# Performance work log

Measured on AMD Instinct MI355X. Metric: run time of the kernel, lower is better.

The kernel has to match this reference:

```python
import jax, jax.numpy as jnp
import numpy as np

TEMPERATURE = 0.07
NORMALIZE = True
NEG_INF = -1e30


def setup_inputs() -> dict:
    key = jax.random.key(0)
    features = jax.random.normal(key, (8192, 512), dtype=jnp.float32)
    return {"features": features}


def reference(features):
    # features: [B, D]
    B = features.shape[0]
    if NORMALIZE:
        norm = jnp.linalg.norm(features, axis=1, keepdims=True)
        features = features / jnp.maximum(norm, 1e-12)
    # [B, B] similarity matrix
    sim = jnp.matmul(features, features.T) / TEMPERATURE

    # default SimCLR labels: arange(B//2) repeated twice -> pair (i, i + B//2)
    half = jnp.arange(B // 2, dtype=jnp.int32)
    labels = jnp.concatenate([half, half])
    eq = labels[None, :] == labels[:, None]          # [B, B]
    diag = jnp.eye(B, dtype=bool)
    mask_pos = eq & ~diag                            # positives per row

    # Original per-row CE: logits = cat(pos_sims, neg_sims) (= all j != i),
    # target index 0 = FIRST positive (lowest column index). Loss_i =
    # logsumexp_{j != i}(sim[i, j]) - sim[i, first_pos_i].
    sim_masked = jnp.where(diag, NEG_INF, sim)
    lse = jax.scipy.special.logsumexp(sim_masked, axis=1)   # [B]

    first_pos = jnp.argmax(mask_pos, axis=1)                 # first True per row
    pos_sim = jnp.take_along_axis(sim, first_pos[:, None], axis=1)[:, 0]

    has_pos = jnp.any(mask_pos, axis=1)
    losses = jnp.where(has_pos, lse - pos_sim, 0.0)
    count = jnp.maximum(jnp.sum(has_pos.astype(jnp.float32)), 1.0)
    return jnp.sum(losses) / count
```

## Files before the change

### kernel.cpp

```cpp
#include <hip/hip_runtime.h>
#include <hip/hip_bf16.h>
#include <stdint.h>

#define BATCH 8192
#define DIM   512
#define TILE  128
#define BK    64
#define NT    (BATCH / TILE)
#define NPAIR (NT * (NT + 1) / 2)

#define FEAT_SCALE 4.5398164f
#define LN2        0.69314718055994531f

typedef __attribute__((ext_vector_type(8))) short short8;
typedef __attribute__((ext_vector_type(4))) float f32x4;

__device__ __forceinline__ void gld_lds16(const void* g, void* l) {
  __builtin_amdgcn_global_load_lds(
      (__attribute__((address_space(1))) void*)(uintptr_t)g,
      (__attribute__((address_space(3))) void*)(uintptr_t)l,
      16, 0, 0);
}

__global__ __launch_bounds__(256) void normalize_bf16(
    const float* __restrict__ x, __hip_bfloat16* __restrict__ o,
    float* __restrict__ rowsum) {
  const int wv = threadIdx.x >> 6, lane = threadIdx.x & 63;
  const int row = blockIdx.x * 4 + wv;
  if (lane == 0) rowsum[row] = 0.0f;
  const float4* xr = (const float4*)(x + (size_t)row * DIM);
  const float4 v0 = xr[lane];
  const float4 v1 = xr[lane + 64];
  float ss = v0.x * v0.x + v0.y * v0.y + v0.z * v0.z + v0.w * v0.w +
             v1.x * v1.x + v1.y * v1.y + v1.z * v1.z + v1.w * v1.w;
#pragma unroll
  for (int m = 32; m > 0; m >>= 1) ss += __shfl_xor(ss, m, 64);
  const float inv = FEAT_SCALE / fmaxf(sqrtf(ss), 1e-12f);
  ushort4 p0, p1;
  p0.x = __bfloat16_as_ushort(__float2bfloat16(v0.x * inv));
  p0.y = __bfloat16_as_ushort(__float2bfloat16(v0.y * inv));
  p0.z = __bfloat16_as_ushort(__float2bfloat16(v0.z * inv));
  p0.w = __bfloat16_as_ushort(__float2bfloat16(v0.w * inv));
  p1.x = __bfloat16_as_ushort(__float2bfloat16(v1.x * inv));
  p1.y = __bfloat16_as_ushort(__float2bfloat16(v1.y * inv));
  p1.z = __bfloat16_as_ushort(__float2bfloat16(v1.z * inv));
  p1.w = __bfloat16_as_ushort(__float2bfloat16(v1.w * inv));
  ushort4* orow = (ushort4*)(o + (size_t)row * DIM);
  orow[lane]      = p0;
  orow[lane + 64] = p1;
}

__global__ __launch_bounds__(256, 4) void sim_lse_kernel(
    const __hip_bfloat16* __restrict__ F, float* __restrict__ rowsum,
    float* __restrict__ possim) {
  __shared__ __hip_bfloat16 smem[2 * TILE * BK];
  __shared__ float colAcc[TILE];

  const int t = blockIdx.x;
  int by = (int)((129.0f - sqrtf(129.0f * 129.0f - 8.0f * (float)t)) * 0.5f);
  if (by > NT - 1) by = NT - 1;
  if (by < 0) by = 0;
  while ((by + 1) * (129 - (by + 1)) / 2 <= t) ++by;
  while (by * (129 - by) / 2 > t) --by;
  const int bx = by + (t - by * (129 - by) / 2);
  const bool diagTile = (bx == by);

  const int rowBase = by * TILE;
  const int colBase = bx * TILE;

  const int tid   = threadIdx.x;
  const int lane  = tid & 63;
  const int wv    = tid >> 6;
  const int waveM = wv >> 1;
  const int waveN = wv & 1;
  const int quad  = lane >> 4;
  const int l15   = lane & 15;

  if (tid < TILE) colAcc[tid] = 0.0f;

  f32x4 acc[4][4] = {};

  const int sb = lane & 7;
  const __hip_bfloat16* gA[4];
  const __hip_bfloat16* gB[4];
  char* ldsA[4];
  char* ldsB[4];
#pragma unroll
  for (int c = 0; c < 4; ++c) {
    const int sRow = wv * 32 + c * 8 + (lane >> 3);
    const int g = sb ^ (sRow & 7);
    gA[c] = F + (size_t)(rowBase + sRow) * DIM + g * 8;
    gB[c] = F + (size_t)(colBase + sRow) * DIM + g * 8;
    ldsA[c] = (char*)smem + (wv * 4 + c) * 1024;
    ldsB[c] = (char*)smem + 16384 + (wv * 4 + c) * 1024;
  }

  int aOff[4], bOff[4];
#pragma unroll
  for (int i = 0; i < 4; ++i) {
    const int Ra = waveM * 64 + i * 16 + l15;
    aOff[i] = Ra * 128 + (quad ^ (Ra & 7)) * 16;
    const int Rb = waveN * 64 + i * 16 + l15;
    bOff[i] = 16384 + Rb * 128 + (quad ^ (Rb & 7)) * 16;
  }
  char* sbase = (char*)smem;

  for (int k0 = 0; k0 < DIM; k0 += BK) {
#pragma unroll
    for (int c = 0; c < 4; ++c) {
      gld_lds16(gA[c] + k0, ldsA[c]);
      gld_lds16(gB[c] + k0, ldsB[c]);
    }
    __syncthreads();

    short8 a[4], b[4];
#pragma unroll
    for (int i = 0; i < 4; ++i) {
      a[i] = *(const short8*)(sbase + aOff[i]);
      b[i] = *(const short8*)(sbase + bOff[i]);
    }
#pragma unroll
    for (int mi = 0; mi < 4; ++mi)
#pragma unroll
      for (int ni = 0; ni < 4; ++ni)
        acc[mi][ni] =
            __builtin_amdgcn_mfma_f32_16x16x32_bf16(a[mi], b[ni], acc[mi][ni], 0, 0, 0);
#pragma unroll
    for (int i = 0; i < 4; ++i) {
      a[i] = *(const short8*)(sbase + (aOff[i] ^ 64));
      b[i] = *(const short8*)(sbase + (bOff[i] ^ 64));
    }
#pragma unroll
    for (int mi = 0; mi < 4; ++mi)
#pragma unroll
      for (int ni = 0; ni < 4; ++ni)
        acc[mi][ni] =
            __builtin_amdgcn_mfma_f32_16x16x32_bf16(a[mi], b[ni], acc[mi][ni], 0, 0, 0);
    __syncthreads();
  }

  float* redBuf = (float*)smem;
  f32x4 rsumv[4] = {};
  float colpart[4] = {0.0f, 0.0f, 0.0f, 0.0f};

  if (diagTile) {
#pragma unroll
    for (int mi = 0; mi < 4; ++mi)
#pragma unroll
      for (int ni = 0; ni < 4; ++ni)
#pragma unroll
        for (int r = 0; r < 4; ++r) {
          const int rl = waveM * 64 + mi * 16 + quad * 4 + r;
          const int cl = waveN * 64 + ni * 16 + l15;
          rsumv[mi][r] += (cl == rl) ? 0.0f : exp2f(acc[mi][ni][r]);
        }
  } else {
    const bool hasPos = (bx == by + 32);
#pragma unroll
    for (int mi = 0; mi < 4; ++mi)
#pragma unroll
      for (int ni = 0; ni < 4; ++ni)
#pragma unroll
        for (int r = 0; r < 4; ++r) {
          const float s = acc[mi][ni][r];
          const float e = exp2f(s);
          rsumv[mi][r] += e;
          colpart[ni] += e;
          if (hasPos) {
            const int rl = waveM * 64 + mi * 16 + quad * 4 + r;
            const int cl = waveN * 64 + ni * 16 + l15;
            if (cl == rl) {
              const int gi = rowBase + rl;
              possim[gi] = s;
              possim[gi + 4096] = s;
            }
          }
        }
  }

  {
    float* wbase = redBuf + ((waveN * 2 + waveM) * 16 + l15) * 68 + quad * 4;
#pragma unroll
    for (int mi = 0; mi < 4; ++mi)
      *(f32x4*)(wbase + mi * 16) = rsumv[mi];
  }

  if (!diagTile) {
#pragma unroll
    for (int ni = 0; ni < 4; ++ni) {
      float c = colpart[ni];
      c += __shfl_xor(c, 16, 64);
      c += __shfl_xor(c, 32, 64);
      if (quad == 0) atomicAdd(&colAcc[waveN * 64 + ni * 16 + l15], c);
    }
  }
  __syncthreads();

  {
    const int wn = tid >> 7, r = tid & 127;
    const int strip = r >> 6, rl = r & 63;
    const float* base = redBuf + ((wn * 2 + strip) * 16) * 68 + rl;
    float s = 0.0f;
#pragma unroll
    for (int j = 0; j < 16; ++j) s += base[j * 68];
    atomicAdd(&rowsum[rowBase + r], s);
  }
  if (tid < TILE && !diagTile)
    atomicAdd(&rowsum[colBase + tid], colAcc[tid]);
}

__global__ __launch_bounds__(1024) void finalize_kernel(
    const float* __restrict__ rowsum, const float* __restrict__ possim,
    float* __restrict__ out) {
  float acc = 0.0f;
  for (int i = threadIdx.x; i < BATCH; i += 1024)
    acc += __logf(rowsum[i]) - possim[i] * LN2;
#pragma unroll
  for (int m = 32; m > 0; m >>= 1) acc += __shfl_xor(acc, m, 64);
  __shared__ float ws[16];
  const int lane = threadIdx.x & 63, wv = threadIdx.x >> 6;
  if (lane == 0) ws[wv] = acc;
  __syncthreads();
  if (threadIdx.x == 0) {
    float tot = 0.0f;
#pragma unroll
    for (int k = 0; k < 16; ++k) tot += ws[k];
    out[0] = tot * (1.0f / (float)BATCH);
  }
}

extern "C" void kernel_launch(void* const* d_in, const int* in_sizes, int n_in,
                              void* d_out, int out_size, void* d_ws, size_t ws_size,
                              hipStream_t stream) {
  const float* x = (const float*)d_in[0];
  float* out = (float*)d_out;

  __hip_bfloat16* Fb = (__hip_bfloat16*)d_ws;
  float* rowsum = (float*)((char*)d_ws + (size_t)BATCH * DIM * sizeof(__hip_bfloat16));
  float* possim = rowsum + BATCH;

  normalize_bf16<<<BATCH / 4, 256, 0, stream>>>(x, Fb, rowsum);
  sim_lse_kernel<<<NPAIR, 256, 0, stream>>>(Fb, rowsum, possim);
  finalize_kernel<<<1, 1024, 0, stream>>>(rowsum, possim, out);
}
```

Before: 112.4 us.

## Use 256x256 tiles with an explicitly pipelined multi-buffered LDS main loop

Doubles the similarity tile to 256x256 and processes it with 512 threads and 8x4 MFMA accumulators per wave, so each loaded row block is reused more and fewer triangular tiles are launched. The K loop is fully unrolled into a hand-scheduled pipeline. Asynchronous global-to-LDS loads for later K slices are issued while MFMAs run on the current slice, using raw s_barrier, vmcnt waits and setprio. The pipeline needs about 129 KB of dynamic LDS, which limits occupancy to one block per CU, and leaves only 528 blocks, which risks load imbalance across CUs.

```diff
diff --git a/kernel.cpp b/kernel.cpp
--- a/kernel.cpp
+++ b/kernel.cpp
@@ -4,9 +4,9 @@
 
 #define BATCH 8192
 #define DIM   512
-#define TILE  128
+#define BM    256
 #define BK    64
-#define NT    (BATCH / TILE)
+#define NT    (BATCH / BM)
 #define NPAIR (NT * (NT + 1) / 2)
 
 #define FEAT_SCALE 4.5398164f
@@ -50,162 +50,178 @@
   orow[lane + 64] = p1;
 }
 
-__global__ __launch_bounds__(256, 4) void sim_lse_kernel(
+__global__ __launch_bounds__(512, 2) void sim_lse_kernel(
     const __hip_bfloat16* __restrict__ F, float* __restrict__ rowsum,
     float* __restrict__ possim) {
-  __shared__ __hip_bfloat16 smem[2 * TILE * BK];
-  __shared__ float colAcc[TILE];
+  extern __shared__ char smem[];
+  float* colAcc = (float*)(smem + 131072);
 
   const int t = blockIdx.x;
-  int by = (int)((129.0f - sqrtf(129.0f * 129.0f - 8.0f * (float)t)) * 0.5f);
+  int by = (int)((65.0f - sqrtf(65.0f * 65.0f - 8.0f * (float)t)) * 0.5f);
   if (by > NT - 1) by = NT - 1;
   if (by < 0) by = 0;
-  while ((by + 1) * (129 - (by + 1)) / 2 <= t) ++by;
-  while (by * (129 - by) / 2 > t) --by;
-  const int bx = by + (t - by * (129 - by) / 2);
+  while ((by + 1) * (65 - (by + 1)) / 2 <= t) ++by;
+  while (by * (65 - by) / 2 > t) --by;
+  const int bx = by + (t - by * (65 - by) / 2);
   const bool diagTile = (bx == by);
-
-  const int rowBase = by * TILE;
-  const int colBase = bx * TILE;
-
-  const int tid   = threadIdx.x;
-  const int lane  = tid & 63;
-  const int wv    = tid >> 6;
-  const int waveM = wv >> 1;
-  const int waveN = wv & 1;
-  const int quad  = lane >> 4;
-  const int l15   = lane & 15;
-
-  if (tid < TILE) colAcc[tid] = 0.0f;
-
-  f32x4 acc[4][4] = {};
-
-  const int sb = lane & 7;
-  const __hip_bfloat16* gA[4];
-  const __hip_bfloat16* gB[4];
-  char* ldsA[4];
-  char* ldsB[4];
-#pragma unroll
-  for (int c = 0; c < 4; ++c) {
-    const int sRow = wv * 32 + c * 8 + (lane >> 3);
-    const int g = sb ^ (sRow & 7);
-    gA[c] = F + (size_t)(rowBase + sRow) * DIM + g * 8;
-    gB[c] = F + (size_t)(colBase + sRow) * DIM + g * 8;
-    ldsA[c] = (char*)smem + (wv * 4 + c) * 1024;
-    ldsB[c] = (char*)smem + 16384 + (wv * 4 + c) * 1024;
-  }
-
-  int aOff[4], bOff[4];
-#pragma unroll
-  for (int i = 0; i < 4; ++i) {
-    const int Ra = waveM * 64 + i * 16 + l15;
-    aOff[i] = Ra * 128 + (quad ^ (Ra & 7)) * 16;
-    const int Rb = waveN * 64 + i * 16 + l15;
-    bOff[i] = 16384 + Rb * 128 + (quad ^ (Rb & 7)) * 16;
-  }
-  char* sbase = (char*)smem;
-
-  for (int k0 = 0; k0 < DIM; k0 += BK) {
-#pragma unroll
-    for (int c = 0; c < 4; ++c) {
-      gld_lds16(gA[c] + k0, ldsA[c]);
-      gld_lds16(gB[c] + k0, ldsB[c]);
+  const bool hasPos = (bx == by + NT / 2);
+
+  const int rowBase = by * BM;
+  const int colBase = bx * BM;
+
+  const int tid  = threadIdx.x;
+  const int lane = tid & 63;
+  const int wv   = tid >> 6;
+  const int q    = lane >> 4;
+  const int l15  = lane & 15;
+  const int waveM = wv >> 2;
+  const int waveN = wv & 3;
+
+  const int r0 = tid >> 2, s0 = tid & 3;
+  const int r1 = (tid + 512) >> 2;
+  const __hip_bfloat16* gA0 = F + (size_t)(rowBase + r0) * DIM + (s0 ^ (r0 & 3)) * 8;
+  const __hip_bfloat16* gA1 = F + (size_t)(rowBase + r1) * DIM + (s0 ^ (r1 & 3)) * 8;
+  const __hip_bfloat16* gB0 = F + (size_t)(colBase + r0) * DIM + (s0 ^ (r0 & 3)) * 8;
+  const __hip_bfloat16* gB1 = F + (size_t)(colBase + r1) * DIM + (s0 ^ (r1 & 3)) * 8;
+  char* ldsW0 = smem + wv * 1024;
+  char* ldsW1 = ldsW0 + 8192;
+
+  const int aoff = waveM * 8192 + l15 * 64 + ((q ^ (l15 & 3)) * 16);
+  const int boff = waveN * 4096 + l15 * 64 + ((q ^ (l15 & 3)) * 16);
+  const char* sA = smem;
+  const char* sB = smem + 65536;
+
+  if (tid < 256) colAcc[tid] = 0.0f;
+
+  f32x4 acc[8][4] = {};
+  short8 a[4], b0[4], b1[4];
+
+#define BARRIER() asm volatile("s_barrier" ::: "memory")
+#define VMCNT4()  asm volatile("s_waitcnt vmcnt(4)" ::: "memory")
+#define SP1() __builtin_amdgcn_s_setprio(1)
+#define SP0() __builtin_amdgcn_s_setprio(0)
+
+#define STAGE(T_, KK_, ISB_) do {                                             \
+    const __hip_bfloat16* g0_ = (ISB_) ? gB0 : gA0;                           \
+    const __hip_bfloat16* g1_ = (ISB_) ? gB1 : gA1;                           \
+    const int ko_ = ((T_) & 7) * BK + (KK_) * 32;                             \
+    const int pl_ = ((((T_) & 1) * 2 + (KK_)) << 14) + ((ISB_) ? 65536 : 0);  \
+    gld_lds16(g0_ + ko_, ldsW0 + pl_);                                        \
+    gld_lds16(g1_ + ko_, ldsW1 + pl_);                                        \
+  } while (0)
+
+#define LDA4(PK_, H_) do {                                                    \
+    const char* p_ = sA + ((PK_) << 14) + aoff + (H_) * 4096;                 \
+    a[0] = *(const short8*)(p_);                                              \
+    a[1] = *(const short8*)(p_ + 1024);                                       \
+    a[2] = *(const short8*)(p_ + 2048);                                       \
+    a[3] = *(const short8*)(p_ + 3072);                                       \
+  } while (0)
+
+#define LDB4(PK_, BV_) do {                                                   \
+    const char* p_ = sB + ((PK_) << 14) + boff;                               \
+    BV_[0] = *(const short8*)(p_);                                            \
+    BV_[1] = *(const short8*)(p_ + 1024);                                     \
+    BV_[2] = *(const short8*)(p_ + 2048);                                     \
+    BV_[3] = *(const short8*)(p_ + 3072);                                     \
+  } while (0)
+
+#define MFMA16(H_, BV_) do {                                                  \
+    _Pragma("unroll")                                                         \
+    for (int m_ = 0; m_ < 4; ++m_)                                            \
+      _Pragma("unroll")                                                       \
+      for (int n_ = 0; n_ < 4; ++n_)                                          \
+        acc[(H_) * 4 + m_][n_] = __builtin_amdgcn_mfma_f32_16x16x32_bf16(     \
+            a[m_], BV_[n_], acc[(H_) * 4 + m_][n_], 0, 0, 0);                 \
+  } while (0)
+
+#define ITER(U_, V_) do {                                                     \
+     LDA4(0, 0); LDB4(0, b0); STAGE((V_), 1, 0);                     \
+    BARRIER(); SP1(); MFMA16(0, b0); SP0(); BARRIER();                        \
+     LDA4(0, 1); STAGE((V_), 1, 1);                                  \
+    BARRIER(); SP1(); MFMA16(1, b0); SP0(); BARRIER();                        \
+     LDA4(1, 0); LDB4(1, b1); STAGE((U_) + 2, 0, 0);                 \
+    BARRIER(); SP1(); MFMA16(0, b1); SP0(); BARRIER();                        \
+     LDA4(1, 1); STAGE((U_) + 2, 0, 1); VMCNT4();                    \
+    BARRIER(); SP1(); MFMA16(1, b1); SP0(); BARRIER();                        \
+     LDA4(2, 0); LDB4(2, b0); STAGE((U_) + 2, 1, 0);                 \
+    BARRIER(); SP1(); MFMA16(0, b0); SP0(); BARRIER();                        \
+     LDA4(2, 1); STAGE((U_) + 2, 1, 1);                              \
+    BARRIER(); SP1(); MFMA16(1, b0); SP0(); BARRIER();                        \
+     LDA4(3, 0); LDB4(3, b1); STAGE((V_) + 2, 0, 0);                 \
+    BARRIER(); SP1(); MFMA16(0, b1); SP0(); BARRIER();                        \
+     LDA4(3, 1); STAGE((V_) + 2, 0, 1); VMCNT4();                    \
+    BARRIER(); SP1(); MFMA16(1, b1); SP0(); BARRIER();                        \
+  } while (0)
+
+  STAGE(0, 0, 0); STAGE(0, 0, 1); STAGE(0, 1, 0); STAGE(0, 1, 1);
+  STAGE(1, 0, 0); STAGE(1, 0, 1);
+  asm volatile("s_waitcnt vmcnt(4) lgkmcnt(0)" ::: "memory");
+  BARRIER();
+
+  ITER(0, 1);
+  ITER(2, 3);
+  ITER(4, 5);
+  ITER(6, 7);
+
+  asm volatile("s_waitcnt vmcnt(0)" ::: "memory");
+  BARRIER();
+
+  float* redBuf = (float*)smem;
+  float cp[4] = {0.f, 0.f, 0.f, 0.f};
+  f32x4 rp[8];
+
+#pragma unroll
+  for (int mi = 0; mi < 8; ++mi) {
+    f32x4 r = {0.f, 0.f, 0.f, 0.f};
+#pragma unroll
+    for (int ni = 0; ni < 4; ++ni) {
+      const int lc = waveN * 64 + ni * 16 + l15;
+#pragma unroll
+      for (int rr = 0; rr < 4; ++rr) {
+        const int lr = waveM * 128 + mi * 16 + q * 4 + rr;
+        const float s = acc[mi][ni][rr];
+        float e = exp2f(s);
+        if (diagTile && lc == lr) e = 0.0f;
+        r[rr] += e;
+        cp[ni] += e;
+        if (hasPos && lc == lr) {
+          const int gi = rowBase + lr;
+          possim[gi] = s;
+          possim[gi + BATCH / 2] = s;
+        }
+      }
     }
-    __syncthreads();
-
-    short8 a[4], b[4];
-#pragma unroll
-    for (int i = 0; i < 4; ++i) {
-      a[i] = *(const short8*)(sbase + aOff[i]);
-      b[i] = *(const short8*)(sbase + bOff[i]);
-    }
-#pragma unroll
-    for (int mi = 0; mi < 4; ++mi)
-#pragma unroll
-      for (int ni = 0; ni < 4; ++ni)
-        acc[mi][ni] =
-            __builtin_amdgcn_mfma_f32_16x16x32_bf16(a[mi], b[ni], acc[mi][ni], 0, 0, 0);
-#pragma unroll
-    for (int i = 0; i < 4; ++i) {
-      a[i] = *(const short8*)(sbase + (aOff[i] ^ 64));
-      b[i] = *(const short8*)(sbase + (bOff[i] ^ 64));
-    }
-#pragma unroll
-    for (int mi = 0; mi < 4; ++mi)
-#pragma unroll
-      for (int ni = 0; ni < 4; ++ni)
-        acc[mi][ni] =
-            __builtin_amdgcn_mfma_f32_16x16x32_bf16(a[mi], b[ni], acc[mi][ni], 0, 0, 0);
-    __syncthreads();
-  }
-
-  float* redBuf = (float*)smem;
-  f32x4 rsumv[4] = {};
-  float colpart[4] = {0.0f, 0.0f, 0.0f, 0.0f};
-
-  if (diagTile) {
-#pragma unroll
-    for (int mi = 0; mi < 4; ++mi)
-#pragma unroll
-      for (int ni = 0; ni < 4; ++ni)
-#pragma unroll
-        for (int r = 0; r < 4; ++r) {
-          const int rl = waveM * 64 + mi * 16 + quad * 4 + r;
-          const int cl = waveN * 64 + ni * 16 + l15;
-          rsumv[mi][r] += (cl == rl) ? 0.0f : exp2f(acc[mi][ni][r]);
-        }
-  } else {
-    const bool hasPos = (bx == by + 32);
-#pragma unroll
-    for (int mi = 0; mi < 4; ++mi)
-#pragma unroll
-      for (int ni = 0; ni < 4; ++ni)
-#pragma unroll
-        for (int r = 0; r < 4; ++r) {
-          const float s = acc[mi][ni][r];
-          const float e = exp2f(s);
-          rsumv[mi][r] += e;
-          colpart[ni] += e;
-          if (hasPos) {
-            const int rl = waveM * 64 + mi * 16 + quad * 4 + r;
-            const int cl = waveN * 64 + ni * 16 + l15;
-            if (cl == rl) {
-              const int gi = rowBase + rl;
-              possim[gi] = s;
-              possim[gi + 4096] = s;
-            }
-          }
-        }
+    rp[mi] = r;
   }
 
   {
-    float* wbase = redBuf + ((waveN * 2 + waveM) * 16 + l15) * 68 + quad * 4;
-#pragma unroll
-    for (int mi = 0; mi < 4; ++mi)
-      *(f32x4*)(wbase + mi * 16) = rsumv[mi];
+    float* wb = redBuf + (waveN * 16 + l15) * 260 + waveM * 128 + q * 4;
+#pragma unroll
+    for (int mi = 0; mi < 8; ++mi) *(f32x4*)(wb + mi * 16) = rp[mi];
   }
 
   if (!diagTile) {
 #pragma unroll
     for (int ni = 0; ni < 4; ++ni) {
-      float c = colpart[ni];
+      float c = cp[ni];
       c += __shfl_xor(c, 16, 64);
       c += __shfl_xor(c, 32, 64);
-      if (quad == 0) atomicAdd(&colAcc[waveN * 64 + ni * 16 + l15], c);
+      if (q == 0) atomicAdd(&colAcc[waveN * 64 + ni * 16 + l15], c);
     }
   }
-  __syncthreads();
+  asm volatile("s_waitcnt lgkmcnt(0)" ::: "memory");
+  BARRIER();
 
   {
-    const int wn = tid >> 7, r = tid & 127;
-    const int strip = r >> 6, rl = r & 63;
-    const float* base = redBuf + ((wn * 2 + strip) * 16) * 68 + rl;
-    float s = 0.0f;
-#pragma unroll
-    for (int j = 0; j < 16; ++j) s += base[j * 68];
-    atomicAdd(&rowsum[rowBase + r], s);
-  }
-  if (tid < TILE && !diagTile)
+    const int row = tid >> 1, half = tid & 1;
+    const float* bp = redBuf + (half * 32) * 260 + row;
+    float ssum = 0.f;
+#pragma unroll
+    for (int j = 0; j < 32; ++j) ssum += bp[j * 260];
+    atomicAdd(&rowsum[rowBase + row], ssum);
+  }
+  if (!diagTile && tid < 256)
     atomicAdd(&rowsum[colBase + tid], colAcc[tid]);
 }
 
@@ -239,7 +255,14 @@
   float* rowsum = (float*)((char*)d_ws + (size_t)BATCH * DIM * sizeof(__hip_bfloat16));
   float* possim = rowsum + BATCH;
 
+  static bool attr_done = false;
+  if (!attr_done) {
+    (void)hipFuncSetAttribute(reinterpret_cast<const void*>(sim_lse_kernel),
+                              hipFuncAttributeMaxDynamicSharedMemorySize, 132096);
+    attr_done = true;
+  }
+
   normalize_bf16<<<BATCH / 4, 256, 0, stream>>>(x, Fb, rowsum);
-  sim_lse_kernel<<<NPAIR, 256, 0, stream>>>(Fb, rowsum, possim);
+  sim_lse_kernel<<<NPAIR, 512, 132096, stream>>>(Fb, rowsum, possim);
   finalize_kernel<<<1, 1024, 0, stream>>>(rowsum, possim, out);
 }
```

Measured after the change: 136.6 us. 21.5% more time.

## Fuse finalize reduction into sim kernel via last-block atomic counter

Applied to the files above, without the earlier changes.

Removes the separate finalize kernel launch. Positive similarities are now summed per tile into a single global accumulator, and the last block to finish, found through an atomic counter with a threadfence, computes the log-sum over row sums and writes the loss. This saves one launch and the per-row possim buffer. In exchange it adds a global atomic and a fence to every block, and the tail reduction runs serially in one 256-thread block.

```diff
diff --git a/kernel.cpp b/kernel.cpp
--- a/kernel.cpp
+++ b/kernel.cpp
@@ -24,10 +24,12 @@
 
 __global__ __launch_bounds__(256) void normalize_bf16(
     const float* __restrict__ x, __hip_bfloat16* __restrict__ o,
-    float* __restrict__ rowsum) {
+    float* __restrict__ rowsum, float* __restrict__ possimSum,
+    int* __restrict__ counter) {
   const int wv = threadIdx.x >> 6, lane = threadIdx.x & 63;
   const int row = blockIdx.x * 4 + wv;
   if (lane == 0) rowsum[row] = 0.0f;
+  if (blockIdx.x == 0 && threadIdx.x == 0) { *possimSum = 0.0f; *counter = 0; }
   const float4* xr = (const float4*)(x + (size_t)row * DIM);
   const float4 v0 = xr[lane];
   const float4 v1 = xr[lane + 64];
@@ -52,9 +54,12 @@
 
 __global__ __launch_bounds__(256, 4) void sim_lse_kernel(
     const __hip_bfloat16* __restrict__ F, float* __restrict__ rowsum,
-    float* __restrict__ possim) {
+    float* __restrict__ possimSum, int* __restrict__ counter,
+    float* __restrict__ out) {
   __shared__ __hip_bfloat16 smem[2 * TILE * BK];
   __shared__ float colAcc[TILE];
+  __shared__ float posSh;
+  __shared__ int lastFlag;
 
   const int t = blockIdx.x;
   int by = (int)((129.0f - sqrtf(129.0f * 129.0f - 8.0f * (float)t)) * 0.5f);
@@ -64,6 +69,7 @@
   while (by * (129 - by) / 2 > t) --by;
   const int bx = by + (t - by * (129 - by) / 2);
   const bool diagTile = (bx == by);
+  const bool hasPos = (bx == by + 32);
 
   const int rowBase = by * TILE;
   const int colBase = bx * TILE;
@@ -77,6 +83,7 @@
   const int l15   = lane & 15;
 
   if (tid < TILE) colAcc[tid] = 0.0f;
+  if (tid == 0) posSh = 0.0f;
 
   f32x4 acc[4][4] = {};
 
@@ -142,6 +149,7 @@
   float* redBuf = (float*)smem;
   f32x4 rsumv[4] = {};
   float colpart[4] = {0.0f, 0.0f, 0.0f, 0.0f};
+  float posAcc = 0.0f;
 
   if (diagTile) {
 #pragma unroll
@@ -155,7 +163,6 @@
           rsumv[mi][r] += (cl == rl) ? 0.0f : exp2f(acc[mi][ni][r]);
         }
   } else {
-    const bool hasPos = (bx == by + 32);
 #pragma unroll
     for (int mi = 0; mi < 4; ++mi)
 #pragma unroll
@@ -169,11 +176,7 @@
           if (hasPos) {
             const int rl = waveM * 64 + mi * 16 + quad * 4 + r;
             const int cl = waveN * 64 + ni * 16 + l15;
-            if (cl == rl) {
-              const int gi = rowBase + rl;
-              possim[gi] = s;
-              possim[gi + 4096] = s;
-            }
+            if (cl == rl) posAcc += s;
           }
         }
   }
@@ -194,6 +197,12 @@
       if (quad == 0) atomicAdd(&colAcc[waveN * 64 + ni * 16 + l15], c);
     }
   }
+  if (hasPos) {
+    float p = posAcc;
+#pragma unroll
+    for (int m = 32; m > 0; m >>= 1) p += __shfl_xor(p, m, 64);
+    if (lane == 0) atomicAdd(&posSh, p);
+  }
   __syncthreads();
 
   {
@@ -207,25 +216,32 @@
   }
   if (tid < TILE && !diagTile)
     atomicAdd(&rowsum[colBase + tid], colAcc[tid]);
-}
-
-__global__ __launch_bounds__(1024) void finalize_kernel(
-    const float* __restrict__ rowsum, const float* __restrict__ possim,
-    float* __restrict__ out) {
-  float acc = 0.0f;
-  for (int i = threadIdx.x; i < BATCH; i += 1024)
-    acc += __logf(rowsum[i]) - possim[i] * LN2;
-#pragma unroll
-  for (int m = 32; m > 0; m >>= 1) acc += __shfl_xor(acc, m, 64);
-  __shared__ float ws[16];
-  const int lane = threadIdx.x & 63, wv = threadIdx.x >> 6;
-  if (lane == 0) ws[wv] = acc;
+  if (tid == 0 && hasPos)
+    atomicAdd(possimSum, 2.0f * posSh);
+
   __syncthreads();
-  if (threadIdx.x == 0) {
-    float tot = 0.0f;
-#pragma unroll
-    for (int k = 0; k < 16; ++k) tot += ws[k];
-    out[0] = tot * (1.0f / (float)BATCH);
+  __threadfence();
+  if (tid == 0)
+    lastFlag = (atomicAdd(counter, 1) == NPAIR - 1) ? 1 : 0;
+  __syncthreads();
+
+  if (lastFlag) {
+    float av = 0.0f;
+    for (int i = tid; i < BATCH; i += 256) {
+      const float rs = __hip_atomic_load(&rowsum[i], __ATOMIC_RELAXED,
+                                         __HIP_MEMORY_SCOPE_AGENT);
+      av += __logf(rs);
+    }
+#pragma unroll
+    for (int m = 32; m > 0; m >>= 1) av += __shfl_xor(av, m, 64);
+    if (lane == 0) colAcc[wv] = av;
+    __syncthreads();
+    if (tid == 0) {
+      const float tot = colAcc[0] + colAcc[1] + colAcc[2] + colAcc[3];
+      const float ps = __hip_atomic_load(possimSum, __ATOMIC_RELAXED,
+                                         __HIP_MEMORY_SCOPE_AGENT);
+      out[0] = (tot - ps * LN2) * (1.0f / (float)BATCH);
+    }
   }
 }
 
@@ -237,9 +253,9 @@
 
   __hip_bfloat16* Fb = (__hip_bfloat16*)d_ws;
   float* rowsum = (float*)((char*)d_ws + (size_t)BATCH * DIM * sizeof(__hip_bfloat16));
-  float* possim = rowsum + BATCH;
-
-  normalize_bf16<<<BATCH / 4, 256, 0, stream>>>(x, Fb, rowsum);
-  sim_lse_kernel<<<NPAIR, 256, 0, stream>>>(Fb, rowsum, possim);
-  finalize_kernel<<<1, 1024, 0, stream>>>(rowsum, possim, out);
-}
+  float* possimSum = rowsum + BATCH;
+  int* counter = (int*)(possimSum + 1);
+
+  normalize_bf16<<<BATCH / 4, 256, 0, stream>>>(x, Fb, rowsum, possimSum, counter);
+  sim_lse_kernel<<<NPAIR, 256, 0, stream>>>(Fb, rowsum, possimSum, counter, out);
+}
```

Result: slower. 260.2 us (+131.6%).
